# Performance work log

Hardware: AMD Instinct MI355X
Metric: run time of the kernel (lower is better)

Reference implementation:

```python
import jax, jax.numpy as jnp
import numpy as np

NSIDE = 128
NPIX = 12 * NSIDE * NSIDE  # 196608
B = 4
FIN = 2
F = 32  # filters


def _cheb_conv(x, idx, w, W, b):
    """Chebyshev graph conv. x:[B,N,Fin], idx:[N,nn] int, w:[N,nn] float,
    W:[K,Fin,Fout], b:[Fout]. T0=x, T1=Lx, Tk=2L T_{k-1}-T_{k-2};
    out = sum_k T_k W_k + b. L is the sparse neighbor-weighted operator."""
    def lap(y):
        # gather neighbor features [B,N,nn,Fc], weighted sum over neighbors
        return jnp.sum(y[:, idx, :] * w[None, :, :, None], axis=2)
    K = W.shape[0]
    out = jnp.einsum('bnf,fo->bno', x, W[0])
    if K > 1:
        Tkm2 = x
        Tkm1 = lap(x)
        out = out + jnp.einsum('bnf,fo->bno', Tkm1, W[1])
        for k in range(2, K):
            Tk = 2.0 * lap(Tkm1) - Tkm2
            out = out + jnp.einsum('bnf,fo->bno', Tk, W[k])
            Tkm2, Tkm1 = Tkm1, Tk
    return out + b


def _layer_norm(x, g, beta, eps=1e-5):
    m = jnp.mean(x, axis=-1, keepdims=True)
    v = jnp.var(x, axis=-1, keepdims=True)
    return (x - m) * jax.lax.rsqrt(v + eps) * g + beta


def _pool4(x):
    # HealPix nested-order pooling: nside -> nside/2, avg over 4 children
    b, n, f = x.shape
    return x.reshape(b, n // 4, 4, f).mean(axis=2)


def _branch(x, idx_a, w_a, Wa, ba, ga, bea, idx_s, w_s, Wb, bb, gb, beb):
    h = _layer_norm(jax.nn.relu(_cheb_conv(x, idx_a, w_a, Wa, ba)), ga, bea)
    h = _pool4(h)  # p=1 nside reduction before the K=2 conv on the coarse graph
    h = _layer_norm(jax.nn.relu(_cheb_conv(h, idx_s, w_s, Wb, bb)), gb, beb)
    return h


def setup_inputs() -> dict:
    key = jax.random.key(0)
    ks = jax.random.split(key, 24)
    d = {}
    d['maps'] = jax.random.normal(ks[0], (B, NPIX, FIN), jnp.float32)
    d['w8'] = jax.random.normal(ks[1], (NPIX, 8), jnp.float32) / 8.0
    d['w20'] = jax.random.normal(ks[2], (NPIX, 20), jnp.float32) / 20.0
    d['w8s'] = jax.random.normal(ks[3], (NPIX // 4, 8), jnp.float32) / 8.0
    d['idx8'] = jax.random.randint(ks[4], (NPIX, 8), 0, NPIX, jnp.int32)
    d['idx20'] = jax.random.randint(ks[5], (NPIX, 20), 0, NPIX, jnp.int32)
    d['idx8s'] = jax.random.randint(ks[6], (NPIX // 4, 8), 0, NPIX // 4, jnp.int32)

    def conv_w(k, K, fin, fout):
        return jax.random.normal(k, (K, fin, fout), jnp.float32) * (1.0 / np.sqrt(K * fin))

    d['W1a'] = conv_w(ks[7], 4, FIN, F);   d['b1a'] = jnp.zeros((F,), jnp.float32)
    d['g1a'] = jnp.ones((F,), jnp.float32); d['be1a'] = jnp.zeros((F,), jnp.float32)
    d['W1b'] = conv_w(ks[8], 2, F, F);     d['b1b'] = jnp.zeros((F,), jnp.float32)
    d['g1b'] = jnp.ones((F,), jnp.float32); d['be1b'] = jnp.zeros((F,), jnp.float32)
    d['W2a'] = conv_w(ks[9], 6, FIN, F);   d['b2a'] = jnp.zeros((F,), jnp.float32)
    d['g2a'] = jnp.ones((F,), jnp.float32); d['be2a'] = jnp.zeros((F,), jnp.float32)
    d['W2b'] = conv_w(ks[10], 2, F, F);    d['b2b'] = jnp.zeros((F,), jnp.float32)
    d['g2b'] = jnp.ones((F,), jnp.float32); d['be2b'] = jnp.zeros((F,), jnp.float32)
    d['W3a'] = conv_w(ks[11], 8, FIN, 2 * F); d['b3a'] = jnp.zeros((2 * F,), jnp.float32)
    d['g3a'] = jnp.ones((2 * F,), jnp.float32); d['be3a'] = jnp.zeros((2 * F,), jnp.float32)
    d['W3b'] = conv_w(ks[12], 2, 2 * F, 2 * F); d['b3b'] = jnp.zeros((2 * F,), jnp.float32)
    d['g3b'] = jnp.ones((2 * F,), jnp.float32); d['be3b'] = jnp.zeros((2 * F,), jnp.float32)
    return d


def reference(maps, w8, w20, w8s, idx8, idx20, idx8s,
              W1a, b1a, g1a, be1a, W1b, b1b, g1b, be1b,
              W2a, b2a, g2a, be2a, W2b, b2b, g2b, be2b,
              W3a, b3a, g3a, be3a, W3b, b3b, g3b, be3b):
    x1 = _branch(maps, idx8, w8, W1a, b1a, g1a, be1a, idx8s, w8s, W1b, b1b, g1b, be1b)
    x2 = _branch(maps, idx8, w8, W2a, b2a, g2a, be2a, idx8s, w8s, W2b, b2b, g2b, be2b)
    x3 = _branch(maps, idx20, w20, W3a, b3a, g3a, be3a, idx8s, w8s, W3b, b3b, g3b, be3b)
    return jnp.concatenate([x1, x2, x3], axis=-1)  # [B, NPIX//4, 4*F]
```

## Files before the change

kernel.cpp:

```cpp
#include <hip/hip_runtime.h>
#include <math.h>

#define NPIXF 196608
#define NCC   49152

typedef unsigned short bfu;
typedef __attribute__((ext_vector_type(8))) short s16x8;
typedef __attribute__((ext_vector_type(4))) float f32x4;

__device__ inline bfu f2bf(float x) {
    union { float f; unsigned u; } v; v.f = x;
    unsigned r = v.u + 0x7fff + ((v.u >> 16) & 1);
    return (bfu)(r >> 16);
}
__device__ inline float bf2f(bfu b) {
    union { unsigned u; float f; } v; v.u = ((unsigned)b) << 16;
    return v.f;
}
__device__ inline float h2f(unsigned short h) {
    _Float16 x; __builtin_memcpy(&x, &h, 2); return (float)x;
}
__device__ inline unsigned short f2h(float f) {
    _Float16 x = (_Float16)f; unsigned short r; __builtin_memcpy(&r, &x, 2); return r;
}
union HPack { uint4 v; unsigned short u[8]; };

template <int NN>
__global__ __launch_bounds__(256) void k_tiw(const int* __restrict__ idx,
                                             const float* __restrict__ w,
                                             int* __restrict__ idxT,
                                             float* __restrict__ wT) {
    int n = blockIdx.x * 256 + threadIdx.x;
    if (n >= NPIXF) return;
#pragma unroll
    for (int j = 0; j < NN; ++j) {
        idxT[j * NPIXF + n] = idx[(size_t)n * NN + j];
        wT[j * NPIXF + n]   = w[(size_t)n * NN + j];
    }
}

__global__ __launch_bounds__(256) void k_transposeH(const float* __restrict__ maps,
                                                    uint4* __restrict__ xtH) {
    int n = blockIdx.x * 256 + threadIdx.x;
    if (n >= NPIXF) return;
    const float2* m2 = (const float2*)maps;
    HPack p;
#pragma unroll
    for (int b = 0; b < 4; ++b) {
        float2 v = m2[(size_t)b * NPIXF + n];
        p.u[2 * b]     = f2h(v.x);
        p.u[2 * b + 1] = f2h(v.y);
    }
    xtH[n] = p.v;
}

template <int NN, bool FIRST>
__global__ __launch_bounds__(256) void k_lapH(const uint4* __restrict__ src,
                                              const uint4* __restrict__ src2,
                                              uint4* __restrict__ dst,
                                              const int* __restrict__ idxT,
                                              const float* __restrict__ wT) {
    int n = blockIdx.x * 256 + threadIdx.x;
    if (n >= NPIXF) return;
    int nj[NN]; float wj[NN];
#pragma unroll
    for (int j = 0; j < NN; ++j) {
        nj[j] = idxT[j * NPIXF + n];
        wj[j] = wT[j * NPIXF + n];
    }
    float a[8] = {0.f, 0.f, 0.f, 0.f, 0.f, 0.f, 0.f, 0.f};
#pragma unroll
    for (int j = 0; j < NN; ++j) {
        HPack x; x.v = src[nj[j]];
#pragma unroll
        for (int e = 0; e < 8; ++e) a[e] = fmaf(wj[j], h2f(x.u[e]), a[e]);
    }
    HPack o;
    if (FIRST) {
#pragma unroll
        for (int e = 0; e < 8; ++e) o.u[e] = f2h(a[e]);
    } else {
        HPack q; q.v = src2[n];
#pragma unroll
        for (int e = 0; e < 8; ++e) o.u[e] = f2h(2.f * a[e] - h2f(q.u[e]));
    }
    dst[n] = o.v;
}

__global__ __launch_bounds__(256) void k_epiA(
    const unsigned* __restrict__ t0, const unsigned* __restrict__ t1,
    const unsigned* __restrict__ t2, const unsigned* __restrict__ t3,
    const unsigned* __restrict__ t4, const unsigned* __restrict__ t5,
    const float* __restrict__ W1a, const float* __restrict__ b1a,
    const float* __restrict__ g1a, const float* __restrict__ be1a,
    const float* __restrict__ W2a, const float* __restrict__ b2a,
    const float* __restrict__ g2a, const float* __restrict__ be2a,
    bfu* __restrict__ h12p) {
    __shared__ float wcA[32 * 24];
    __shared__ float tvlds[4 * 64 * 12];
    __shared__ float mrA[256 * 4];

    int tid = threadIdx.x;
    if (tid < 64) {
        int kk = tid >> 3, f4 = (tid & 7) * 4;
        float4 v = *(const float4*)(W1a + kk * 32 + f4);
        wcA[(f4 + 0) * 24 + kk] = v.x; wcA[(f4 + 1) * 24 + kk] = v.y;
        wcA[(f4 + 2) * 24 + kk] = v.z; wcA[(f4 + 3) * 24 + kk] = v.w;
    } else if (tid < 160) {
        int u = tid - 64;
        int kk = u >> 3, f4 = (u & 7) * 4;
        float4 v = *(const float4*)(W2a + kk * 32 + f4);
        wcA[(f4 + 0) * 24 + 8 + kk] = v.x; wcA[(f4 + 1) * 24 + 8 + kk] = v.y;
        wcA[(f4 + 2) * 24 + 8 + kk] = v.z; wcA[(f4 + 3) * 24 + 8 + kk] = v.w;
    } else if (tid < 192) {
        wcA[(tid - 160) * 24 + 20] = b1a[tid - 160];
    } else if (tid < 224) {
        wcA[(tid - 192) * 24 + 21] = b2a[tid - 192];
    }
    __syncthreads();

    int lane = tid & 63;
    int wv = tid >> 6;
    int b = lane & 3;
    int n = blockIdx.x * 64 + wv * 16 + (lane >> 2);

    float tv[12];
    {
        const unsigned* tp[6] = {t0, t1, t2, t3, t4, t5};
#pragma unroll
        for (int t = 0; t < 6; ++t) {
            unsigned v = tp[t][n * 4 + b];
            tv[2 * t]     = h2f((unsigned short)(v & 0xffff));
            tv[2 * t + 1] = h2f((unsigned short)(v >> 16));
        }
    }
    float* tvw = tvlds + wv * (64 * 12);
    {
        float4* d4 = (float4*)(tvw + lane * 12);
        d4[0] = make_float4(tv[0], tv[1], tv[2], tv[3]);
        d4[1] = make_float4(tv[4], tv[5], tv[6], tv[7]);
        d4[2] = make_float4(tv[8], tv[9], tv[10], tv[11]);
    }
    float s1 = 0.f, q1 = 0.f, s2 = 0.f, q2 = 0.f;
#pragma unroll 4
    for (int f = 0; f < 32; ++f) {
        const float* wc = wcA + f * 24;
        const float4 u0 = *(const float4*)(wc + 0), u1 = *(const float4*)(wc + 4);
        const float4 v0 = *(const float4*)(wc + 8), v1 = *(const float4*)(wc + 12),
                     v2 = *(const float4*)(wc + 16);
        float o1 = wc[20];
        o1 = fmaf(tv[0], u0.x, o1); o1 = fmaf(tv[1], u0.y, o1);
        o1 = fmaf(tv[2], u0.z, o1); o1 = fmaf(tv[3], u0.w, o1);
        o1 = fmaf(tv[4], u1.x, o1); o1 = fmaf(tv[5], u1.y, o1);
        o1 = fmaf(tv[6], u1.z, o1); o1 = fmaf(tv[7], u1.w, o1);
        o1 = fmaxf(o1, 0.f);
        float o2 = wc[21];
        o2 = fmaf(tv[0], v0.x, o2); o2 = fmaf(tv[1], v0.y, o2);
        o2 = fmaf(tv[2], v0.z, o2); o2 = fmaf(tv[3], v0.w, o2);
        o2 = fmaf(tv[4], v1.x, o2); o2 = fmaf(tv[5], v1.y, o2);
        o2 = fmaf(tv[6], v1.z, o2); o2 = fmaf(tv[7], v1.w, o2);
        o2 = fmaf(tv[8], v2.x, o2); o2 = fmaf(tv[9], v2.y, o2);
        o2 = fmaf(tv[10], v2.z, o2); o2 = fmaf(tv[11], v2.w, o2);
        o2 = fmaxf(o2, 0.f);
        s1 += o1; q1 = fmaf(o1, o1, q1);
        s2 += o2; q2 = fmaf(o2, o2, q2);
    }
    {
        float m1 = s1 * 0.03125f, va1 = q1 * 0.03125f - m1 * m1;
        float m2 = s2 * 0.03125f, va2 = q2 * 0.03125f - m2 * m2;
        *(float4*)(mrA + (wv * 64 + lane) * 4) =
            make_float4(m1, rsqrtf(va1 + 1e-5f), m2, rsqrtf(va2 + 1e-5f));
    }

    int f = lane & 31;
    int br = lane >> 5;
    float wreg[12];
#pragma unroll
    for (int k = 0; k < 12; ++k) {
        float w1v = (k < 8) ? W1a[k * 32 + f] : 0.f;
        wreg[k] = br ? W2a[k * 32 + f] : w1v;
    }
    float bb = br ? b2a[f] : b1a[f];
    float gg = br ? g2a[f] : g1a[f];
    float bt = br ? be2a[f] : be1a[f];
    int C0 = blockIdx.x * 16 + wv * 4;
#pragma unroll
    for (int cl = 0; cl < 4; ++cl) {
#pragma unroll
        for (int b2 = 0; b2 < 4; ++b2) {
            float acc = 0.f;
#pragma unroll
            for (int j = 0; j < 4; ++j) {
                int cb = (cl * 4 + j) * 4 + b2;
                const float* tp = tvw + cb * 12;
                const float4 a0 = *(const float4*)(tp + 0);
                const float4 a1 = *(const float4*)(tp + 4);
                const float4 a2 = *(const float4*)(tp + 8);
                float o = bb;
                o = fmaf(a0.x, wreg[0], o); o = fmaf(a0.y, wreg[1], o);
                o = fmaf(a0.z, wreg[2], o); o = fmaf(a0.w, wreg[3], o);
                o = fmaf(a1.x, wreg[4], o); o = fmaf(a1.y, wreg[5], o);
                o = fmaf(a1.z, wreg[6], o); o = fmaf(a1.w, wreg[7], o);
                o = fmaf(a2.x, wreg[8], o); o = fmaf(a2.y, wreg[9], o);
                o = fmaf(a2.z, wreg[10], o); o = fmaf(a2.w, wreg[11], o);
                o = fmaxf(o, 0.f);
                const float4 mr4 = *(const float4*)(mrA + (wv * 64 + cb) * 4);
                float m = br ? mr4.z : mr4.x;
                float r = br ? mr4.w : mr4.y;
                acc += fmaf((o - m) * r, gg, bt);
            }
            h12p[((size_t)(C0 + cl) * 4 + b2) * 64 + br * 32 + f] = f2bf(acc * 0.25f);
        }
    }
}

__global__ __launch_bounds__(256) void k_epiB(
    const unsigned* __restrict__ t0, const unsigned* __restrict__ t1,
    const unsigned* __restrict__ t2, const unsigned* __restrict__ t3,
    const unsigned* __restrict__ t4, const unsigned* __restrict__ t5,
    const unsigned* __restrict__ t6, const unsigned* __restrict__ t7,
    const float* __restrict__ W3a, const float* __restrict__ b3a,
    const float* __restrict__ g3a, const float* __restrict__ be3a,
    bfu* __restrict__ h3p) {
    __shared__ float wcol[64 * 20];
    __shared__ float tvlds[4 * 64 * 20];
    __shared__ float mr[256 * 2];

    int tid = threadIdx.x;
    {
        int kk = tid >> 4, f4 = (tid & 15) * 4;
        float4 v = *(const float4*)(W3a + kk * 64 + f4);
        wcol[(f4 + 0) * 20 + kk] = v.x; wcol[(f4 + 1) * 20 + kk] = v.y;
        wcol[(f4 + 2) * 20 + kk] = v.z; wcol[(f4 + 3) * 20 + kk] = v.w;
        if (tid < 64) wcol[tid * 20 + 16] = b3a[tid];
    }
    __syncthreads();

    int lane = tid & 63;
    int wv = tid >> 6;
    int b = lane & 3;
    int n = blockIdx.x * 64 + wv * 16 + (lane >> 2);

    float tv[16];
    {
        const unsigned* tp[8] = {t0, t1, t2, t3, t4, t5, t6, t7};
#pragma unroll
        for (int t = 0; t < 8; ++t) {
            unsigned v = tp[t][n * 4 + b];
            tv[2 * t]     = h2f((unsigned short)(v & 0xffff));
            tv[2 * t + 1] = h2f((unsigned short)(v >> 16));
        }
    }
    float* tvw = tvlds + wv * (64 * 20);
    {
        float4* d4 = (float4*)(tvw + lane * 20);
        d4[0] = make_float4(tv[0], tv[1], tv[2], tv[3]);
        d4[1] = make_float4(tv[4], tv[5], tv[6], tv[7]);
        d4[2] = make_float4(tv[8], tv[9], tv[10], tv[11]);
        d4[3] = make_float4(tv[12], tv[13], tv[14], tv[15]);
    }
    float s = 0.f, q = 0.f;
#pragma unroll 4
    for (int f = 0; f < 64; ++f) {
        const float* wc = wcol + f * 20;
        const float4 w0 = *(const float4*)(wc + 0), w1 = *(const float4*)(wc + 4);
        const float4 w2 = *(const float4*)(wc + 8), w3 = *(const float4*)(wc + 12);
        float o = wc[16];
        o = fmaf(tv[0], w0.x, o);  o = fmaf(tv[1], w0.y, o);
        o = fmaf(tv[2], w0.z, o);  o = fmaf(tv[3], w0.w, o);
        o = fmaf(tv[4], w1.x, o);  o = fmaf(tv[5], w1.y, o);
        o = fmaf(tv[6], w1.z, o);  o = fmaf(tv[7], w1.w, o);
        o = fmaf(tv[8], w2.x, o);  o = fmaf(tv[9], w2.y, o);
        o = fmaf(tv[10], w2.z, o); o = fmaf(tv[11], w2.w, o);
        o = fmaf(tv[12], w3.x, o); o = fmaf(tv[13], w3.y, o);
        o = fmaf(tv[14], w3.z, o); o = fmaf(tv[15], w3.w, o);
        o = fmaxf(o, 0.f);
        s += o; q = fmaf(o, o, q);
    }
    {
        float m = s * 0.015625f;
        float va = q * 0.015625f - m * m;
        *(float2*)(mr + (wv * 64 + lane) * 2) = make_float2(m, rsqrtf(va + 1e-5f));
    }

    float wreg[16];
#pragma unroll
    for (int k = 0; k < 16; ++k) wreg[k] = W3a[k * 64 + lane];
    float bb = b3a[lane], gg = g3a[lane], bt = be3a[lane];
    int C0 = blockIdx.x * 16 + wv * 4;
#pragma unroll
    for (int cl = 0; cl < 4; ++cl) {
#pragma unroll
        for (int b2 = 0; b2 < 4; ++b2) {
            float acc = 0.f;
#pragma unroll
            for (int j = 0; j < 4; ++j) {
                int cb = (cl * 4 + j) * 4 + b2;
                const float* tp = tvw + cb * 20;
                const float4 a0 = *(const float4*)(tp + 0);
                const float4 a1 = *(const float4*)(tp + 4);
                const float4 a2 = *(const float4*)(tp + 8);
                const float4 a3 = *(const float4*)(tp + 12);
                float o = bb;
                o = fmaf(a0.x, wreg[0], o);  o = fmaf(a0.y, wreg[1], o);
                o = fmaf(a0.z, wreg[2], o);  o = fmaf(a0.w, wreg[3], o);
                o = fmaf(a1.x, wreg[4], o);  o = fmaf(a1.y, wreg[5], o);
                o = fmaf(a1.z, wreg[6], o);  o = fmaf(a1.w, wreg[7], o);
                o = fmaf(a2.x, wreg[8], o);  o = fmaf(a2.y, wreg[9], o);
                o = fmaf(a2.z, wreg[10], o); o = fmaf(a2.w, wreg[11], o);
                o = fmaf(a3.x, wreg[12], o); o = fmaf(a3.y, wreg[13], o);
                o = fmaf(a3.z, wreg[14], o); o = fmaf(a3.w, wreg[15], o);
                o = fmaxf(o, 0.f);
                const float2 mrv = *(const float2*)(mr + (wv * 64 + cb) * 2);
                acc += fmaf((o - mrv.x) * mrv.y, gg, bt);
            }
            h3p[((size_t)(C0 + cl) * 4 + b2) * 64 + lane] = f2bf(acc * 0.25f);
        }
    }
}

__device__ __constant__ const int s12arr[8] = {0, 1, 0, 1, 2, 3, 2, 3};
__device__ __constant__ const int t12arr[8] = {0, 0, 1, 1, 2, 2, 3, 3};

__global__ __launch_bounds__(256) void k_wprep(
    const float* __restrict__ W3b, const float* __restrict__ W1b,
    const float* __restrict__ W2b, uint4* __restrict__ Wfrag3,
    uint4* __restrict__ Wfrag12) {
    int e = blockIdx.x * 256 + threadIdx.x;
    union { uint4 v; bfu u[8]; } p;
    if (e < 1024) {
        int st = e >> 6, l = e & 63;
        int s = st >> 2, t = st & 3, g = l >> 4, c = l & 15;
#pragma unroll
        for (int j = 0; j < 8; ++j) {
            int k = 32 * s + 8 * g + j;
            int col = 16 * t + c;
            float wv = (k < 64) ? W3b[k * 64 + col] : W3b[4096 + (k - 64) * 64 + col];
            p.u[j] = f2bf(wv);
        }
        Wfrag3[e] = p.v;
    } else if (e < 1536) {
        int ee = e - 1024;
        int fi = ee >> 6, l = ee & 63;
        int s = s12arr[fi], t = t12arr[fi], g = l >> 4, c = l & 15;
#pragma unroll
        for (int j = 0; j < 8; ++j) {
            int k = 32 * s + 8 * g + j;
            float wv;
            if (t < 2) {
                int col = 16 * t + c;
                wv = (k < 32) ? W1b[k * 32 + col] : W1b[1024 + (k - 32) * 32 + col];
            } else {
                int f2 = 16 * (t - 2) + c;
                int kk = k - 64;
                wv = (kk < 32) ? W2b[kk * 32 + f2] : W2b[1024 + (kk - 32) * 32 + f2];
            }
            p.u[j] = f2bf(wv);
        }
        Wfrag12[ee] = p.v;
    }
}

__global__ __launch_bounds__(256) void k_coarse3m(
    const bfu* __restrict__ h3, const int* __restrict__ idx, const float* __restrict__ w,
    const uint4* __restrict__ Wfrag3, const float* __restrict__ b3b,
    const float* __restrict__ g3b, const float* __restrict__ be3b,
    float* __restrict__ out) {
    __shared__ bfu alds[4][16][136];
    int tid = threadIdx.x;
    int lane = tid & 63;
    int wv = tid >> 6;
    int g = lane >> 4, cL = lane & 15;
    int c0 = blockIdx.x * 16 + wv * 4;

    int iv = 0; float wvv = 0.f;
    if (lane < 32) {
        iv = idx[(c0 + (lane >> 3)) * 8 + (lane & 7)];
        wvv = w[(c0 + (lane >> 3)) * 8 + (lane & 7)];
    }
    const ushort4* hb = (const ushort4*)h3;
#pragma unroll
    for (int cl = 0; cl < 4; ++cl) {
        ushort4 v0 = hb[(size_t)(c0 + cl) * 64 + lane];
        float a0 = 0.f, a1 = 0.f, a2 = 0.f, a3 = 0.f;
#pragma unroll
        for (int j = 0; j < 8; ++j) {
            int nj = __shfl(iv, cl * 8 + j);
            float wj = __shfl(wvv, cl * 8 + j);
            ushort4 x = hb[(size_t)nj * 64 + lane];
            a0 = fmaf(wj, bf2f(x.x), a0);
            a1 = fmaf(wj, bf2f(x.y), a1);
            a2 = fmaf(wj, bf2f(x.z), a2);
            a3 = fmaf(wj, bf2f(x.w), a3);
        }
        int r = cl * 4 + g;
        *(ushort4*)&alds[wv][r][4 * cL] = v0;
        ushort4 p;
        p.x = f2bf(a0); p.y = f2bf(a1); p.z = f2bf(a2); p.w = f2bf(a3);
        *(ushort4*)&alds[wv][r][64 + 4 * cL] = p;
    }

    f32x4 acc[4];
#pragma unroll
    for (int t = 0; t < 4; ++t) {
        float bs = b3b[16 * t + cL];
        acc[t] = (f32x4){bs, bs, bs, bs};
    }
    s16x8 af[4];
#pragma unroll
    for (int s = 0; s < 4; ++s)
        af[s] = *(const s16x8*)&alds[wv][cL][32 * s + 8 * g];
#pragma unroll
    for (int s = 0; s < 4; ++s) {
#pragma unroll
        for (int t = 0; t < 4; ++t) {
            s16x8 bf = *(const s16x8*)&Wfrag3[(s * 4 + t) * 64 + lane];
            acc[t] = __builtin_amdgcn_mfma_f32_16x16x32_bf16(af[s], bf, acc[t], 0, 0, 0);
        }
    }

    float s_[4] = {0.f, 0.f, 0.f, 0.f}, q_[4] = {0.f, 0.f, 0.f, 0.f};
#pragma unroll
    for (int t = 0; t < 4; ++t)
#pragma unroll
        for (int j = 0; j < 4; ++j) {
            float o = fmaxf(acc[t][j], 0.f);
            acc[t][j] = o;
            s_[j] += o; q_[j] = fmaf(o, o, q_[j]);
        }
#pragma unroll
    for (int m = 1; m < 16; m <<= 1)
#pragma unroll
        for (int j = 0; j < 4; ++j) {
            s_[j] += __shfl_xor(s_[j], m, 16);
            q_[j] += __shfl_xor(q_[j], m, 16);
        }
    float mu[4], rs[4];
#pragma unroll
    for (int j = 0; j < 4; ++j) {
        mu[j] = s_[j] * 0.015625f;
        float va = q_[j] * 0.015625f - mu[j] * mu[j];
        rs[j] = rsqrtf(va + 1e-5f);
    }
#pragma unroll
    for (int t = 0; t < 4; ++t) {
        float gg = g3b[16 * t + cL], bt = be3b[16 * t + cL];
#pragma unroll
        for (int j = 0; j < 4; ++j) {
            int r = 4 * g + j;
            int cl = r >> 2, b = r & 3;
            out[((size_t)b * NCC + c0 + cl) * 128 + 64 + 16 * t + cL] =
                fmaf((acc[t][j] - mu[j]) * rs[j], gg, bt);
        }
    }
}

__global__ __launch_bounds__(256) void k_coarse12m(
    const bfu* __restrict__ h12, const int* __restrict__ idx, const float* __restrict__ w,
    const uint4* __restrict__ Wfrag12,
    const float* __restrict__ b1b, const float* __restrict__ g1b, const float* __restrict__ be1b,
    const float* __restrict__ b2b, const float* __restrict__ g2b, const float* __restrict__ be2b,
    float* __restrict__ out) {
    __shared__ bfu alds[4][16][136];
    int tid = threadIdx.x;
    int lane = tid & 63;
    int wv = tid >> 6;
    int g = lane >> 4, cL = lane & 15;
    int c0 = blockIdx.x * 16 + wv * 4;

    int iv = 0; float wvv = 0.f;
    if (lane < 32) {
        iv = idx[(c0 + (lane >> 3)) * 8 + (lane & 7)];
        wvv = w[(c0 + (lane >> 3)) * 8 + (lane & 7)];
    }
    const ushort4* hb = (const ushort4*)h12;
    int k0 = (cL < 8) ? 4 * cL : 32 + 4 * cL;
#pragma unroll
    for (int cl = 0; cl < 4; ++cl) {
        ushort4 v0 = hb[(size_t)(c0 + cl) * 64 + lane];
        float a0 = 0.f, a1 = 0.f, a2 = 0.f, a3 = 0.f;
#pragma unroll
        for (int j = 0; j < 8; ++j) {
            int nj = __shfl(iv, cl * 8 + j);
            float wj = __shfl(wvv, cl * 8 + j);
            ushort4 x = hb[(size_t)nj * 64 + lane];
            a0 = fmaf(wj, bf2f(x.x), a0);
            a1 = fmaf(wj, bf2f(x.y), a1);
            a2 = fmaf(wj, bf2f(x.z), a2);
            a3 = fmaf(wj, bf2f(x.w), a3);
        }
        int r = cl * 4 + g;
        *(ushort4*)&alds[wv][r][k0] = v0;
        ushort4 p;
        p.x = f2bf(a0); p.y = f2bf(a1); p.z = f2bf(a2); p.w = f2bf(a3);
        *(ushort4*)&alds[wv][r][k0 + 32] = p;
    }

    f32x4 acc[4];
#pragma unroll
    for (int t = 0; t < 4; ++t) {
        float bs = (t < 2) ? b1b[16 * t + cL] : b2b[16 * (t - 2) + cL];
        acc[t] = (f32x4){bs, bs, bs, bs};
    }
    s16x8 af[4];
#pragma unroll
    for (int s = 0; s < 4; ++s)
        af[s] = *(const s16x8*)&alds[wv][cL][32 * s + 8 * g];
#pragma unroll
    for (int fi = 0; fi < 8; ++fi) {
        int s = s12arr[fi], t = t12arr[fi];
        s16x8 bf = *(const s16x8*)&Wfrag12[fi * 64 + lane];
        acc[t] = __builtin_amdgcn_mfma_f32_16x16x32_bf16(af[s], bf, acc[t], 0, 0, 0);
    }

    float sb[2][4], qb[2][4];
#pragma unroll
    for (int br = 0; br < 2; ++br)
#pragma unroll
        for (int j = 0; j < 4; ++j) { sb[br][j] = 0.f; qb[br][j] = 0.f; }
#pragma unroll
    for (int t = 0; t < 4; ++t) {
        int br = t >> 1;
#pragma unroll
        for (int j = 0; j < 4; ++j) {
            float o = fmaxf(acc[t][j], 0.f);
            acc[t][j] = o;
            sb[br][j] += o; qb[br][j] = fmaf(o, o, qb[br][j]);
        }
    }
#pragma unroll
    for (int m = 1; m < 16; m <<= 1)
#pragma unroll
        for (int br = 0; br < 2; ++br)
#pragma unroll
            for (int j = 0; j < 4; ++j) {
                sb[br][j] += __shfl_xor(sb[br][j], m, 16);
                qb[br][j] += __shfl_xor(qb[br][j], m, 16);
            }
    float mu[2][4], rs[2][4];
#pragma unroll
    for (int br = 0; br < 2; ++br)
#pragma unroll
        for (int j = 0; j < 4; ++j) {
            mu[br][j] = sb[br][j] * 0.03125f;
            float va = qb[br][j] * 0.03125f - mu[br][j] * mu[br][j];
            rs[br][j] = rsqrtf(va + 1e-5f);
        }
#pragma unroll
    for (int t = 0; t < 4; ++t) {
        int br = t >> 1;
        float gg = (t < 2) ? g1b[16 * t + cL] : g2b[16 * (t - 2) + cL];
        float bt = (t < 2) ? be1b[16 * t + cL] : be2b[16 * (t - 2) + cL];
#pragma unroll
        for (int j = 0; j < 4; ++j) {
            int r = 4 * g + j;
            int cl = r >> 2, b = r & 3;
            out[((size_t)b * NCC + c0 + cl) * 128 + 16 * t + cL] =
                fmaf((acc[t][j] - mu[br][j]) * rs[br][j], gg, bt);
        }
    }
}

extern "C" void kernel_launch(void* const* d_in, const int* in_sizes, int n_in,
                              void* d_out, int out_size, void* d_ws, size_t ws_size,
                              hipStream_t stream) {
    const float* maps = (const float*)d_in[0];
    const float* w8   = (const float*)d_in[1];
    const float* w20  = (const float*)d_in[2];
    const float* w8s  = (const float*)d_in[3];
    const int*   idx8  = (const int*)d_in[4];
    const int*   idx20 = (const int*)d_in[5];
    const int*   idx8s = (const int*)d_in[6];
    const float* W1a = (const float*)d_in[7];
    const float* b1a = (const float*)d_in[8];
    const float* g1a = (const float*)d_in[9];
    const float* be1a = (const float*)d_in[10];
    const float* W1b = (const float*)d_in[11];
    const float* b1b = (const float*)d_in[12];
    const float* g1b = (const float*)d_in[13];
    const float* be1b = (const float*)d_in[14];
    const float* W2a = (const float*)d_in[15];
    const float* b2a = (const float*)d_in[16];
    const float* g2a = (const float*)d_in[17];
    const float* be2a = (const float*)d_in[18];
    const float* W2b = (const float*)d_in[19];
    const float* b2b = (const float*)d_in[20];
    const float* g2b = (const float*)d_in[21];
    const float* be2b = (const float*)d_in[22];
    const float* W3a = (const float*)d_in[23];
    const float* b3a = (const float*)d_in[24];
    const float* g3a = (const float*)d_in[25];
    const float* be3a = (const float*)d_in[26];
    const float* W3b = (const float*)d_in[27];
    const float* b3b = (const float*)d_in[28];
    const float* g3b = (const float*)d_in[29];
    const float* be3b = (const float*)d_in[30];
    float* out = (float*)d_out;

    float* ws = (float*)d_ws;
    uint4* xtH = (uint4*)ws;
    uint4* slot[7];
    for (int i = 0; i < 7; ++i) slot[i] = (uint4*)(ws + (size_t)786432 * (1 + i));
    bfu* h12p = (bfu*)(ws + (size_t)12582912);
    bfu* h3p  = (bfu*)(ws + (size_t)18874368);
    int*   idx8T  = (int*)(ws + 12582912);
    float* w8T    = ws + 12582912 + 1572864;
    int*   idx20T = (int*)(ws + 25165824);
    float* w20T   = ws + 29097984;
    uint4* Wfrag3  = (uint4*)(ws + 33030144);
    uint4* Wfrag12 = (uint4*)(ws + 33034240);

    dim3 blk(256);
    dim3 gN(NPIXF / 256);
    dim3 gE(NPIXF / 64);
    dim3 gC(NCC / 16);

    k_wprep<<<6, blk, 0, stream>>>(W3b, W1b, W2b, Wfrag3, Wfrag12);
    k_tiw<8><<<gN, blk, 0, stream>>>(idx8, w8, idx8T, w8T);
    k_tiw<20><<<gN, blk, 0, stream>>>(idx20, w20, idx20T, w20T);
    k_transposeH<<<gN, blk, 0, stream>>>(maps, xtH);

    k_lapH<8, true><<<gN, blk, 0, stream>>>(xtH, xtH, slot[0], idx8T, w8T);
    k_lapH<8, false><<<gN, blk, 0, stream>>>(slot[0], xtH, slot[1], idx8T, w8T);
    k_lapH<8, false><<<gN, blk, 0, stream>>>(slot[1], slot[0], slot[2], idx8T, w8T);
    k_lapH<8, false><<<gN, blk, 0, stream>>>(slot[2], slot[1], slot[3], idx8T, w8T);
    k_lapH<8, false><<<gN, blk, 0, stream>>>(slot[3], slot[2], slot[4], idx8T, w8T);

    k_epiA<<<gE, blk, 0, stream>>>((const unsigned*)xtH, (const unsigned*)slot[0],
                                   (const unsigned*)slot[1], (const unsigned*)slot[2],
                                   (const unsigned*)slot[3], (const unsigned*)slot[4],
                                   W1a, b1a, g1a, be1a, W2a, b2a, g2a, be2a, h12p);

    k_lapH<20, true><<<gN, blk, 0, stream>>>(xtH, xtH, slot[0], idx20T, w20T);
    k_lapH<20, false><<<gN, blk, 0, stream>>>(slot[0], xtH, slot[1], idx20T, w20T);
    k_lapH<20, false><<<gN, blk, 0, stream>>>(slot[1], slot[0], slot[2], idx20T, w20T);
    k_lapH<20, false><<<gN, blk, 0, stream>>>(slot[2], slot[1], slot[3], idx20T, w20T);
    k_lapH<20, false><<<gN, blk, 0, stream>>>(slot[3], slot[2], slot[4], idx20T, w20T);
    k_lapH<20, false><<<gN, blk, 0, stream>>>(slot[4], slot[3], slot[5], idx20T, w20T);
    k_lapH<20, false><<<gN, blk, 0, stream>>>(slot[5], slot[4], slot[6], idx20T, w20T);

    k_epiB<<<gE, blk, 0, stream>>>((const unsigned*)xtH, (const unsigned*)slot[0],
                                   (const unsigned*)slot[1], (const unsigned*)slot[2],
                                   (const unsigned*)slot[3], (const unsigned*)slot[4],
                                   (const unsigned*)slot[5], (const unsigned*)slot[6],
                                   W3a, b3a, g3a, be3a, h3p);

    k_coarse12m<<<gC, blk, 0, stream>>>(h12p, idx8s, w8s, Wfrag12,
                                        b1b, g1b, be1b, b2b, g2b, be2b, out);
    k_coarse3m<<<gC, blk, 0, stream>>>(h3p, idx8s, w8s, Wfrag3, b3b, g3b, be3b, out);
}
```

Before: 596.8 us.

## Move fine-level conv epilogues onto bf16 MFMA with shuffle-based layer norm

Replaces the scalar FMA epilogue kernels (Chebyshev combine, ReLU, layer norm, pool) with MFMA 16x16x32 bf16 versions. Weight fragments are pre-packed in the weight-prep kernel, and each wave handles one coarse pixel (16 rows). Mean and variance are reduced with lane shuffles and the 4-child pool with cross-group shuffles. This cuts VALU work and LDS traffic but lowers the T-term inputs from fp16 to bf16 precision.

```diff
diff --git a/kernel.cpp b/kernel.cpp
--- a/kernel.cpp
+++ b/kernel.cpp
@@ -87,245 +87,15 @@
     dst[n] = o.v;
 }
 
-__global__ __launch_bounds__(256) void k_epiA(
-    const unsigned* __restrict__ t0, const unsigned* __restrict__ t1,
-    const unsigned* __restrict__ t2, const unsigned* __restrict__ t3,
-    const unsigned* __restrict__ t4, const unsigned* __restrict__ t5,
-    const float* __restrict__ W1a, const float* __restrict__ b1a,
-    const float* __restrict__ g1a, const float* __restrict__ be1a,
-    const float* __restrict__ W2a, const float* __restrict__ b2a,
-    const float* __restrict__ g2a, const float* __restrict__ be2a,
-    bfu* __restrict__ h12p) {
-    __shared__ float wcA[32 * 24];
-    __shared__ float tvlds[4 * 64 * 12];
-    __shared__ float mrA[256 * 4];
-
-    int tid = threadIdx.x;
-    if (tid < 64) {
-        int kk = tid >> 3, f4 = (tid & 7) * 4;
-        float4 v = *(const float4*)(W1a + kk * 32 + f4);
-        wcA[(f4 + 0) * 24 + kk] = v.x; wcA[(f4 + 1) * 24 + kk] = v.y;
-        wcA[(f4 + 2) * 24 + kk] = v.z; wcA[(f4 + 3) * 24 + kk] = v.w;
-    } else if (tid < 160) {
-        int u = tid - 64;
-        int kk = u >> 3, f4 = (u & 7) * 4;
-        float4 v = *(const float4*)(W2a + kk * 32 + f4);
-        wcA[(f4 + 0) * 24 + 8 + kk] = v.x; wcA[(f4 + 1) * 24 + 8 + kk] = v.y;
-        wcA[(f4 + 2) * 24 + 8 + kk] = v.z; wcA[(f4 + 3) * 24 + 8 + kk] = v.w;
-    } else if (tid < 192) {
-        wcA[(tid - 160) * 24 + 20] = b1a[tid - 160];
-    } else if (tid < 224) {
-        wcA[(tid - 192) * 24 + 21] = b2a[tid - 192];
-    }
-    __syncthreads();
-
-    int lane = tid & 63;
-    int wv = tid >> 6;
-    int b = lane & 3;
-    int n = blockIdx.x * 64 + wv * 16 + (lane >> 2);
-
-    float tv[12];
-    {
-        const unsigned* tp[6] = {t0, t1, t2, t3, t4, t5};
-#pragma unroll
-        for (int t = 0; t < 6; ++t) {
-            unsigned v = tp[t][n * 4 + b];
-            tv[2 * t]     = h2f((unsigned short)(v & 0xffff));
-            tv[2 * t + 1] = h2f((unsigned short)(v >> 16));
-        }
-    }
-    float* tvw = tvlds + wv * (64 * 12);
-    {
-        float4* d4 = (float4*)(tvw + lane * 12);
-        d4[0] = make_float4(tv[0], tv[1], tv[2], tv[3]);
-        d4[1] = make_float4(tv[4], tv[5], tv[6], tv[7]);
-        d4[2] = make_float4(tv[8], tv[9], tv[10], tv[11]);
-    }
-    float s1 = 0.f, q1 = 0.f, s2 = 0.f, q2 = 0.f;
-#pragma unroll 4
-    for (int f = 0; f < 32; ++f) {
-        const float* wc = wcA + f * 24;
-        const float4 u0 = *(const float4*)(wc + 0), u1 = *(const float4*)(wc + 4);
-        const float4 v0 = *(const float4*)(wc + 8), v1 = *(const float4*)(wc + 12),
-                     v2 = *(const float4*)(wc + 16);
-        float o1 = wc[20];
-        o1 = fmaf(tv[0], u0.x, o1); o1 = fmaf(tv[1], u0.y, o1);
-        o1 = fmaf(tv[2], u0.z, o1); o1 = fmaf(tv[3], u0.w, o1);
-        o1 = fmaf(tv[4], u1.x, o1); o1 = fmaf(tv[5], u1.y, o1);
-        o1 = fmaf(tv[6], u1.z, o1); o1 = fmaf(tv[7], u1.w, o1);
-        o1 = fmaxf(o1, 0.f);
-        float o2 = wc[21];
-        o2 = fmaf(tv[0], v0.x, o2); o2 = fmaf(tv[1], v0.y, o2);
-        o2 = fmaf(tv[2], v0.z, o2); o2 = fmaf(tv[3], v0.w, o2);
-        o2 = fmaf(tv[4], v1.x, o2); o2 = fmaf(tv[5], v1.y, o2);
-        o2 = fmaf(tv[6], v1.z, o2); o2 = fmaf(tv[7], v1.w, o2);
-        o2 = fmaf(tv[8], v2.x, o2); o2 = fmaf(tv[9], v2.y, o2);
-        o2 = fmaf(tv[10], v2.z, o2); o2 = fmaf(tv[11], v2.w, o2);
-        o2 = fmaxf(o2, 0.f);
-        s1 += o1; q1 = fmaf(o1, o1, q1);
-        s2 += o2; q2 = fmaf(o2, o2, q2);
-    }
-    {
-        float m1 = s1 * 0.03125f, va1 = q1 * 0.03125f - m1 * m1;
-        float m2 = s2 * 0.03125f, va2 = q2 * 0.03125f - m2 * m2;
-        *(float4*)(mrA + (wv * 64 + lane) * 4) =
-            make_float4(m1, rsqrtf(va1 + 1e-5f), m2, rsqrtf(va2 + 1e-5f));
-    }
-
-    int f = lane & 31;
-    int br = lane >> 5;
-    float wreg[12];
-#pragma unroll
-    for (int k = 0; k < 12; ++k) {
-        float w1v = (k < 8) ? W1a[k * 32 + f] : 0.f;
-        wreg[k] = br ? W2a[k * 32 + f] : w1v;
-    }
-    float bb = br ? b2a[f] : b1a[f];
-    float gg = br ? g2a[f] : g1a[f];
-    float bt = br ? be2a[f] : be1a[f];
-    int C0 = blockIdx.x * 16 + wv * 4;
-#pragma unroll
-    for (int cl = 0; cl < 4; ++cl) {
-#pragma unroll
-        for (int b2 = 0; b2 < 4; ++b2) {
-            float acc = 0.f;
-#pragma unroll
-            for (int j = 0; j < 4; ++j) {
-                int cb = (cl * 4 + j) * 4 + b2;
-                const float* tp = tvw + cb * 12;
-                const float4 a0 = *(const float4*)(tp + 0);
-                const float4 a1 = *(const float4*)(tp + 4);
-                const float4 a2 = *(const float4*)(tp + 8);
-                float o = bb;
-                o = fmaf(a0.x, wreg[0], o); o = fmaf(a0.y, wreg[1], o);
-                o = fmaf(a0.z, wreg[2], o); o = fmaf(a0.w, wreg[3], o);
-                o = fmaf(a1.x, wreg[4], o); o = fmaf(a1.y, wreg[5], o);
-                o = fmaf(a1.z, wreg[6], o); o = fmaf(a1.w, wreg[7], o);
-                o = fmaf(a2.x, wreg[8], o); o = fmaf(a2.y, wreg[9], o);
-                o = fmaf(a2.z, wreg[10], o); o = fmaf(a2.w, wreg[11], o);
-                o = fmaxf(o, 0.f);
-                const float4 mr4 = *(const float4*)(mrA + (wv * 64 + cb) * 4);
-                float m = br ? mr4.z : mr4.x;
-                float r = br ? mr4.w : mr4.y;
-                acc += fmaf((o - m) * r, gg, bt);
-            }
-            h12p[((size_t)(C0 + cl) * 4 + b2) * 64 + br * 32 + f] = f2bf(acc * 0.25f);
-        }
-    }
-}
-
-__global__ __launch_bounds__(256) void k_epiB(
-    const unsigned* __restrict__ t0, const unsigned* __restrict__ t1,
-    const unsigned* __restrict__ t2, const unsigned* __restrict__ t3,
-    const unsigned* __restrict__ t4, const unsigned* __restrict__ t5,
-    const unsigned* __restrict__ t6, const unsigned* __restrict__ t7,
-    const float* __restrict__ W3a, const float* __restrict__ b3a,
-    const float* __restrict__ g3a, const float* __restrict__ be3a,
-    bfu* __restrict__ h3p) {
-    __shared__ float wcol[64 * 20];
-    __shared__ float tvlds[4 * 64 * 20];
-    __shared__ float mr[256 * 2];
-
-    int tid = threadIdx.x;
-    {
-        int kk = tid >> 4, f4 = (tid & 15) * 4;
-        float4 v = *(const float4*)(W3a + kk * 64 + f4);
-        wcol[(f4 + 0) * 20 + kk] = v.x; wcol[(f4 + 1) * 20 + kk] = v.y;
-        wcol[(f4 + 2) * 20 + kk] = v.z; wcol[(f4 + 3) * 20 + kk] = v.w;
-        if (tid < 64) wcol[tid * 20 + 16] = b3a[tid];
-    }
-    __syncthreads();
-
-    int lane = tid & 63;
-    int wv = tid >> 6;
-    int b = lane & 3;
-    int n = blockIdx.x * 64 + wv * 16 + (lane >> 2);
-
-    float tv[16];
-    {
-        const unsigned* tp[8] = {t0, t1, t2, t3, t4, t5, t6, t7};
-#pragma unroll
-        for (int t = 0; t < 8; ++t) {
-            unsigned v = tp[t][n * 4 + b];
-            tv[2 * t]     = h2f((unsigned short)(v & 0xffff));
-            tv[2 * t + 1] = h2f((unsigned short)(v >> 16));
-        }
-    }
-    float* tvw = tvlds + wv * (64 * 20);
-    {
-        float4* d4 = (float4*)(tvw + lane * 20);
-        d4[0] = make_float4(tv[0], tv[1], tv[2], tv[3]);
-        d4[1] = make_float4(tv[4], tv[5], tv[6], tv[7]);
-        d4[2] = make_float4(tv[8], tv[9], tv[10], tv[11]);
-        d4[3] = make_float4(tv[12], tv[13], tv[14], tv[15]);
-    }
-    float s = 0.f, q = 0.f;
-#pragma unroll 4
-    for (int f = 0; f < 64; ++f) {
-        const float* wc = wcol + f * 20;
-        const float4 w0 = *(const float4*)(wc + 0), w1 = *(const float4*)(wc + 4);
-        const float4 w2 = *(const float4*)(wc + 8), w3 = *(const float4*)(wc + 12);
-        float o = wc[16];
-        o = fmaf(tv[0], w0.x, o);  o = fmaf(tv[1], w0.y, o);
-        o = fmaf(tv[2], w0.z, o);  o = fmaf(tv[3], w0.w, o);
-        o = fmaf(tv[4], w1.x, o);  o = fmaf(tv[5], w1.y, o);
-        o = fmaf(tv[6], w1.z, o);  o = fmaf(tv[7], w1.w, o);
-        o = fmaf(tv[8], w2.x, o);  o = fmaf(tv[9], w2.y, o);
-        o = fmaf(tv[10], w2.z, o); o = fmaf(tv[11], w2.w, o);
-        o = fmaf(tv[12], w3.x, o); o = fmaf(tv[13], w3.y, o);
-        o = fmaf(tv[14], w3.z, o); o = fmaf(tv[15], w3.w, o);
-        o = fmaxf(o, 0.f);
-        s += o; q = fmaf(o, o, q);
-    }
-    {
-        float m = s * 0.015625f;
-        float va = q * 0.015625f - m * m;
-        *(float2*)(mr + (wv * 64 + lane) * 2) = make_float2(m, rsqrtf(va + 1e-5f));
-    }
-
-    float wreg[16];
-#pragma unroll
-    for (int k = 0; k < 16; ++k) wreg[k] = W3a[k * 64 + lane];
-    float bb = b3a[lane], gg = g3a[lane], bt = be3a[lane];
-    int C0 = blockIdx.x * 16 + wv * 4;
-#pragma unroll
-    for (int cl = 0; cl < 4; ++cl) {
-#pragma unroll
-        for (int b2 = 0; b2 < 4; ++b2) {
-            float acc = 0.f;
-#pragma unroll
-            for (int j = 0; j < 4; ++j) {
-                int cb = (cl * 4 + j) * 4 + b2;
-                const float* tp = tvw + cb * 20;
-                const float4 a0 = *(const float4*)(tp + 0);
-                const float4 a1 = *(const float4*)(tp + 4);
-                const float4 a2 = *(const float4*)(tp + 8);
-                const float4 a3 = *(const float4*)(tp + 12);
-                float o = bb;
-                o = fmaf(a0.x, wreg[0], o);  o = fmaf(a0.y, wreg[1], o);
-                o = fmaf(a0.z, wreg[2], o);  o = fmaf(a0.w, wreg[3], o);
-                o = fmaf(a1.x, wreg[4], o);  o = fmaf(a1.y, wreg[5], o);
-                o = fmaf(a1.z, wreg[6], o);  o = fmaf(a1.w, wreg[7], o);
-                o = fmaf(a2.x, wreg[8], o);  o = fmaf(a2.y, wreg[9], o);
-                o = fmaf(a2.z, wreg[10], o); o = fmaf(a2.w, wreg[11], o);
-                o = fmaf(a3.x, wreg[12], o); o = fmaf(a3.y, wreg[13], o);
-                o = fmaf(a3.z, wreg[14], o); o = fmaf(a3.w, wreg[15], o);
-                o = fmaxf(o, 0.f);
-                const float2 mrv = *(const float2*)(mr + (wv * 64 + cb) * 2);
-                acc += fmaf((o - mrv.x) * mrv.y, gg, bt);
-            }
-            h3p[((size_t)(C0 + cl) * 4 + b2) * 64 + lane] = f2bf(acc * 0.25f);
-        }
-    }
-}
-
 __device__ __constant__ const int s12arr[8] = {0, 1, 0, 1, 2, 3, 2, 3};
 __device__ __constant__ const int t12arr[8] = {0, 0, 1, 1, 2, 2, 3, 3};
 
 __global__ __launch_bounds__(256) void k_wprep(
     const float* __restrict__ W3b, const float* __restrict__ W1b,
-    const float* __restrict__ W2b, uint4* __restrict__ Wfrag3,
-    uint4* __restrict__ Wfrag12) {
+    const float* __restrict__ W2b, const float* __restrict__ W3a,
+    const float* __restrict__ W1a, const float* __restrict__ W2a,
+    uint4* __restrict__ Wfrag3, uint4* __restrict__ Wfrag12,
+    uint4* __restrict__ WfragE3, uint4* __restrict__ WfragE12) {
     int e = blockIdx.x * 256 + threadIdx.x;
     union { uint4 v; bfu u[8]; } p;
     if (e < 1024) {
@@ -358,6 +128,215 @@
             p.u[j] = f2bf(wv);
         }
         Wfrag12[ee] = p.v;
+    } else if (e < 1792) {
+        int ee = e - 1536;
+        int t = ee >> 6, l = ee & 63;
+        int g = l >> 4, c = l & 15;
+#pragma unroll
+        for (int j = 0; j < 8; ++j) {
+            int k = 8 * g + j;
+            float wv = (k < 16) ? W3a[k * 64 + 16 * t + c] : 0.f;
+            p.u[j] = f2bf(wv);
+        }
+        WfragE3[ee] = p.v;
+    } else if (e < 2048) {
+        int ee = e - 1792;
+        int t = ee >> 6, l = ee & 63;
+        int g = l >> 4, c = l & 15;
+        int col = 16 * t + c;
+#pragma unroll
+        for (int j = 0; j < 8; ++j) {
+            int k = 8 * g + j;
+            float wv = 0.f;
+            if (col < 32) { if (k < 8)  wv = W1a[k * 32 + col]; }
+            else          { if (k < 12) wv = W2a[k * 32 + (col - 32)]; }
+            p.u[j] = f2bf(wv);
+        }
+        WfragE12[ee] = p.v;
+    }
+}
+
+__global__ __launch_bounds__(256) void k_epiAm(
+    const unsigned* __restrict__ t0, const unsigned* __restrict__ t1,
+    const unsigned* __restrict__ t2, const unsigned* __restrict__ t3,
+    const unsigned* __restrict__ t4, const unsigned* __restrict__ t5,
+    const uint4* __restrict__ WfragE12,
+    const float* __restrict__ b1a, const float* __restrict__ g1a,
+    const float* __restrict__ be1a,
+    const float* __restrict__ b2a, const float* __restrict__ g2a,
+    const float* __restrict__ be2a,
+    bfu* __restrict__ h12p) {
+    __shared__ bfu alds[4][16][34];
+    int tid = threadIdx.x;
+    int lane = tid & 63;
+    int wv = tid >> 6;
+    int c = blockIdx.x * 4 + wv;
+    int r = lane & 15, q = lane >> 4;
+
+    union { uint4 v; bfu u[8]; } pk;
+    if (q == 0) {
+        int uidx = 16 * c + r;
+        unsigned v0 = t0[uidx], v1 = t1[uidx], v2 = t2[uidx], v3 = t3[uidx];
+        pk.u[0] = f2bf(h2f((unsigned short)(v0 & 0xffff)));
+        pk.u[1] = f2bf(h2f((unsigned short)(v0 >> 16)));
+        pk.u[2] = f2bf(h2f((unsigned short)(v1 & 0xffff)));
+        pk.u[3] = f2bf(h2f((unsigned short)(v1 >> 16)));
+        pk.u[4] = f2bf(h2f((unsigned short)(v2 & 0xffff)));
+        pk.u[5] = f2bf(h2f((unsigned short)(v2 >> 16)));
+        pk.u[6] = f2bf(h2f((unsigned short)(v3 & 0xffff)));
+        pk.u[7] = f2bf(h2f((unsigned short)(v3 >> 16)));
+    } else if (q == 1) {
+        int uidx = 16 * c + r;
+        unsigned v4 = t4[uidx], v5 = t5[uidx];
+        pk.u[0] = f2bf(h2f((unsigned short)(v4 & 0xffff)));
+        pk.u[1] = f2bf(h2f((unsigned short)(v4 >> 16)));
+        pk.u[2] = f2bf(h2f((unsigned short)(v5 & 0xffff)));
+        pk.u[3] = f2bf(h2f((unsigned short)(v5 >> 16)));
+        pk.u[4] = 0; pk.u[5] = 0; pk.u[6] = 0; pk.u[7] = 0;
+    } else {
+        pk.u[0] = 0; pk.u[1] = 0; pk.u[2] = 0; pk.u[3] = 0;
+        pk.u[4] = 0; pk.u[5] = 0; pk.u[6] = 0; pk.u[7] = 0;
+    }
+    *(uint4*)&alds[wv][r][8 * q] = pk.v;
+
+    int cL = lane & 15, g = lane >> 4;
+    f32x4 acc[4];
+#pragma unroll
+    for (int t = 0; t < 4; ++t) {
+        int f = 16 * t + cL;
+        float bs = (t < 2) ? b1a[f] : b2a[f - 32];
+        acc[t] = (f32x4){bs, bs, bs, bs};
+    }
+    s16x8 af = *(const s16x8*)&alds[wv][cL][8 * g];
+#pragma unroll
+    for (int t = 0; t < 4; ++t) {
+        s16x8 bf = *(const s16x8*)&WfragE12[t * 64 + lane];
+        acc[t] = __builtin_amdgcn_mfma_f32_16x16x32_bf16(af, bf, acc[t], 0, 0, 0);
+    }
+
+    float sb[2][4], qb[2][4];
+#pragma unroll
+    for (int br = 0; br < 2; ++br)
+#pragma unroll
+        for (int j = 0; j < 4; ++j) { sb[br][j] = 0.f; qb[br][j] = 0.f; }
+#pragma unroll
+    for (int t = 0; t < 4; ++t) {
+        int br = t >> 1;
+#pragma unroll
+        for (int j = 0; j < 4; ++j) {
+            float o = fmaxf(acc[t][j], 0.f);
+            acc[t][j] = o;
+            sb[br][j] += o; qb[br][j] = fmaf(o, o, qb[br][j]);
+        }
+    }
+#pragma unroll
+    for (int m = 1; m < 16; m <<= 1)
+#pragma unroll
+        for (int br = 0; br < 2; ++br)
+#pragma unroll
+            for (int j = 0; j < 4; ++j) {
+                sb[br][j] += __shfl_xor(sb[br][j], m, 16);
+                qb[br][j] += __shfl_xor(qb[br][j], m, 16);
+            }
+#pragma unroll
+    for (int t = 0; t < 4; ++t) {
+        int br = t >> 1;
+        int f = 16 * t + cL;
+        float gg = (t < 2) ? g1a[f] : g2a[f - 32];
+        float bt = (t < 2) ? be1a[f] : be2a[f - 32];
+#pragma unroll
+        for (int j = 0; j < 4; ++j) {
+            float mu = sb[br][j] * 0.03125f;
+            float va = qb[br][j] * 0.03125f - mu * mu;
+            float v = fmaf((acc[t][j] - mu) * rsqrtf(va + 1e-5f), gg, bt);
+            v += __shfl_xor(v, 16, 64);
+            v += __shfl_xor(v, 32, 64);
+            if (g == t)
+                h12p[((size_t)c * 4 + j) * 64 + f] = f2bf(v * 0.25f);
+        }
+    }
+}
+
+__global__ __launch_bounds__(256) void k_epiBm(
+    const unsigned* __restrict__ t0, const unsigned* __restrict__ t1,
+    const unsigned* __restrict__ t2, const unsigned* __restrict__ t3,
+    const unsigned* __restrict__ t4, const unsigned* __restrict__ t5,
+    const unsigned* __restrict__ t6, const unsigned* __restrict__ t7,
+    const uint4* __restrict__ WfragE3,
+    const float* __restrict__ b3a, const float* __restrict__ g3a,
+    const float* __restrict__ be3a,
+    bfu* __restrict__ h3p) {
+    __shared__ bfu alds[4][16][34];
+    int tid = threadIdx.x;
+    int lane = tid & 63;
+    int wv = tid >> 6;
+    int c = blockIdx.x * 4 + wv;
+    int r = lane & 15, q = lane >> 4;
+
+    union { uint4 v; bfu u[8]; } pk;
+    if (q < 2) {
+        int uidx = 16 * c + r;
+        unsigned v0, v1, v2, v3;
+        if (q == 0) { v0 = t0[uidx]; v1 = t1[uidx]; v2 = t2[uidx]; v3 = t3[uidx]; }
+        else        { v0 = t4[uidx]; v1 = t5[uidx]; v2 = t6[uidx]; v3 = t7[uidx]; }
+        pk.u[0] = f2bf(h2f((unsigned short)(v0 & 0xffff)));
+        pk.u[1] = f2bf(h2f((unsigned short)(v0 >> 16)));
+        pk.u[2] = f2bf(h2f((unsigned short)(v1 & 0xffff)));
+        pk.u[3] = f2bf(h2f((unsigned short)(v1 >> 16)));
+        pk.u[4] = f2bf(h2f((unsigned short)(v2 & 0xffff)));
+        pk.u[5] = f2bf(h2f((unsigned short)(v2 >> 16)));
+        pk.u[6] = f2bf(h2f((unsigned short)(v3 & 0xffff)));
+        pk.u[7] = f2bf(h2f((unsigned short)(v3 >> 16)));
+    } else {
+        pk.u[0] = 0; pk.u[1] = 0; pk.u[2] = 0; pk.u[3] = 0;
+        pk.u[4] = 0; pk.u[5] = 0; pk.u[6] = 0; pk.u[7] = 0;
+    }
+    *(uint4*)&alds[wv][r][8 * q] = pk.v;
+
+    int cL = lane & 15, g = lane >> 4;
+    f32x4 acc[4];
+#pragma unroll
+    for (int t = 0; t < 4; ++t) {
+        float bs = b3a[16 * t + cL];
+        acc[t] = (f32x4){bs, bs, bs, bs};
+    }
+    s16x8 af = *(const s16x8*)&alds[wv][cL][8 * g];
+#pragma unroll
+    for (int t = 0; t < 4; ++t) {
+        s16x8 bf = *(const s16x8*)&WfragE3[t * 64 + lane];
+        acc[t] = __builtin_amdgcn_mfma_f32_16x16x32_bf16(af, bf, acc[t], 0, 0, 0);
+    }
+
+    float s_[4] = {0.f, 0.f, 0.f, 0.f}, q_[4] = {0.f, 0.f, 0.f, 0.f};
+#pragma unroll
+    for (int t = 0; t < 4; ++t)
+#pragma unroll
+        for (int j = 0; j < 4; ++j) {
+            float o = fmaxf(acc[t][j], 0.f);
+            acc[t][j] = o;
+            s_[j] += o; q_[j] = fmaf(o, o, q_[j]);
+        }
+#pragma unroll
+    for (int m = 1; m < 16; m <<= 1)
+#pragma unroll
+        for (int j = 0; j < 4; ++j) {
+            s_[j] += __shfl_xor(s_[j], m, 16);
+            q_[j] += __shfl_xor(q_[j], m, 16);
+        }
+#pragma unroll
+    for (int t = 0; t < 4; ++t) {
+        int f = 16 * t + cL;
+        float gg = g3a[f], bt = be3a[f];
+#pragma unroll
+        for (int j = 0; j < 4; ++j) {
+            float mu = s_[j] * 0.015625f;
+            float va = q_[j] * 0.015625f - mu * mu;
+            float v = fmaf((acc[t][j] - mu) * rsqrtf(va + 1e-5f), gg, bt);
+            v += __shfl_xor(v, 16, 64);
+            v += __shfl_xor(v, 32, 64);
+            if (g == t)
+                h3p[((size_t)c * 4 + j) * 64 + f] = f2bf(v * 0.25f);
+        }
     }
 }
 
@@ -607,15 +586,18 @@
     float* w8T    = ws + 12582912 + 1572864;
     int*   idx20T = (int*)(ws + 25165824);
     float* w20T   = ws + 29097984;
-    uint4* Wfrag3  = (uint4*)(ws + 33030144);
-    uint4* Wfrag12 = (uint4*)(ws + 33034240);
+    uint4* Wfrag3   = (uint4*)(ws + 33030144);
+    uint4* Wfrag12  = (uint4*)(ws + 33034240);
+    uint4* WfragE3  = (uint4*)(ws + 33036288);
+    uint4* WfragE12 = (uint4*)(ws + 33037312);
 
     dim3 blk(256);
     dim3 gN(NPIXF / 256);
-    dim3 gE(NPIXF / 64);
+    dim3 gEm(NCC / 4);
     dim3 gC(NCC / 16);
 
-    k_wprep<<<6, blk, 0, stream>>>(W3b, W1b, W2b, Wfrag3, Wfrag12);
+    k_wprep<<<8, blk, 0, stream>>>(W3b, W1b, W2b, W3a, W1a, W2a,
+                                   Wfrag3, Wfrag12, WfragE3, WfragE12);
     k_tiw<8><<<gN, blk, 0, stream>>>(idx8, w8, idx8T, w8T);
     k_tiw<20><<<gN, blk, 0, stream>>>(idx20, w20, idx20T, w20T);
     k_transposeH<<<gN, blk, 0, stream>>>(maps, xtH);
@@ -626,10 +608,10 @@
     k_lapH<8, false><<<gN, blk, 0, stream>>>(slot[2], slot[1], slot[3], idx8T, w8T);
     k_lapH<8, false><<<gN, blk, 0, stream>>>(slot[3], slot[2], slot[4], idx8T, w8T);
 
-    k_epiA<<<gE, blk, 0, stream>>>((const unsigned*)xtH, (const unsigned*)slot[0],
-                                   (const unsigned*)slot[1], (const unsigned*)slot[2],
-                                   (const unsigned*)slot[3], (const unsigned*)slot[4],
-                                   W1a, b1a, g1a, be1a, W2a, b2a, g2a, be2a, h12p);
+    k_epiAm<<<gEm, blk, 0, stream>>>((const unsigned*)xtH, (const unsigned*)slot[0],
+                                     (const unsigned*)slot[1], (const unsigned*)slot[2],
+                                     (const unsigned*)slot[3], (const unsigned*)slot[4],
+                                     WfragE12, b1a, g1a, be1a, b2a, g2a, be2a, h12p);
 
     k_lapH<20, true><<<gN, blk, 0, stream>>>(xtH, xtH, slot[0], idx20T, w20T);
     k_lapH<20, false><<<gN, blk, 0, stream>>>(slot[0], xtH, slot[1], idx20T, w20T);
@@ -639,11 +621,11 @@
     k_lapH<20, false><<<gN, blk, 0, stream>>>(slot[4], slot[3], slot[5], idx20T, w20T);
     k_lapH<20, false><<<gN, blk, 0, stream>>>(slot[5], slot[4], slot[6], idx20T, w20T);
 
-    k_epiB<<<gE, blk, 0, stream>>>((const unsigned*)xtH, (const unsigned*)slot[0],
-                                   (const unsigned*)slot[1], (const unsigned*)slot[2],
-                                   (const unsigned*)slot[3], (const unsigned*)slot[4],
-                                   (const unsigned*)slot[5], (const unsigned*)slot[6],
-                                   W3a, b3a, g3a, be3a, h3p);
+    k_epiBm<<<gEm, blk, 0, stream>>>((const unsigned*)xtH, (const unsigned*)slot[0],
+                                     (const unsigned*)slot[1], (const unsigned*)slot[2],
+                                     (const unsigned*)slot[3], (const unsigned*)slot[4],
+                                     (const unsigned*)slot[5], (const unsigned*)slot[6],
+                                     WfragE3, b3a, g3a, be3a, h3p);
 
     k_coarse12m<<<gC, blk, 0, stream>>>(h12p, idx8s, w8s, Wfrag12,
                                         b1b, g1b, be1b, b2b, g2b, be2b, out);
```

Result: faster. 583.6 us (-2.2%).
